# Kernel optimization log

Hardware: AMD Instinct MI355X
Metric: run time of the kernel (lower is better)

Reference implementation:

```python
import jax, jax.numpy as jnp
import numpy as np

N = 64      # num_neighbors + 1
H = 512     # hidden_size
T = 1024    # history length


def setup_inputs() -> dict:
    key = jax.random.key(0)
    ks = jax.random.split(key, 10)
    s = 1.0 / np.sqrt(H)  # PyTorch LSTM/Linear init scale
    return {
        "in_recent_values": jax.random.normal(ks[0], (N,), dtype=jnp.float32),
        "in_reputation_history": jax.random.normal(ks[1], (N, T), dtype=jnp.float32),
        # per-module LSTM params (input_size=1), gate order i,f,g,o
        "W_ih": jax.random.uniform(ks[2], (N, 4 * H), jnp.float32, -s, s),      # [N,4H] (input_size=1 squeezed)
        "W_hh": jax.random.uniform(ks[3], (N, 4 * H, H), jnp.float32, -s, s),   # [N,4H,H]
        "b_ih": jax.random.uniform(ks[4], (N, 4 * H), jnp.float32, -s, s),
        "b_hh": jax.random.uniform(ks[5], (N, 4 * H), jnp.float32, -s, s),
        # per-module output Linear(H+1 -> 1)
        "lin_W": jax.random.uniform(ks[6], (N, H + 1), jnp.float32, -s, s),
        "lin_b": jax.random.uniform(ks[7], (N,), jnp.float32, -s, s),
        # final Linear(N -> 1)
        "final_W": jax.random.uniform(ks[8], (N,), jnp.float32, -1.0 / np.sqrt(N), 1.0 / np.sqrt(N)),
        "final_b": jax.random.uniform(ks[9], (1,), jnp.float32, -1.0 / np.sqrt(N), 1.0 / np.sqrt(N)),
    }


def _batched_lstm_last_h(history, W_ih, W_hh, b_ih, b_hh):
    # history: [N,T]. Precompute input contribution for all steps: [T,N,4H]
    x_proj = history[:, :, None] * W_ih[:, None, :] + (b_ih + b_hh)[:, None, :]
    x_proj = jnp.swapaxes(x_proj, 0, 1)  # [T,N,4H]

    def step(carry, x_t):
        h, c = carry  # [N,H] each
        gates = x_t + jnp.einsum("nh,ngh->ng", h, W_hh)  # [N,4H]
        i, f, g, o = jnp.split(gates, 4, axis=-1)
        i = jax.nn.sigmoid(i)
        f = jax.nn.sigmoid(f)
        g = jnp.tanh(g)
        o = jax.nn.sigmoid(o)
        c = f * c + i * g
        h = o * jnp.tanh(c)
        return (h, c), None

    h0 = jnp.zeros((N, H), dtype=history.dtype)
    (h_last, _), _ = jax.lax.scan(step, (h0, h0), x_proj)
    return h_last  # [N,H]


def reference(in_recent_values, in_reputation_history, W_ih, W_hh, b_ih, b_hh,
              lin_W, lin_b, final_W, final_b):
    h_last = _batched_lstm_last_h(in_reputation_history, W_ih, W_hh, b_ih, b_hh)
    # per-module linear on [h_last, current_reading] -> scalar each
    feat = jnp.concatenate([h_last, in_recent_values[:, None]], axis=1)  # [N,H+1]
    per_mod = jnp.sum(feat * lin_W, axis=1) + lin_b                      # [N]
    out = per_mod @ final_W + final_b                                    # [1]
    return out
```

## Files before the change

### kernel.cpp

```cpp
#include <hip/hip_runtime.h>
#include <hip/hip_fp16.h>
#include <cstddef>

#define NMOD 64
#define HID 512
#define TSTEPS 1024
#define G4 2048

#define WOFF_PERMOD 0
#define WOFF_HX     16384
#define WOFF_W16    524288
#define W16_BYTES   ((size_t)NMOD * G4 * HID * 2)
#define WS_NEED     (WOFF_W16 + W16_BYTES)

typedef _Float16 h2_t __attribute__((ext_vector_type(2)));
union U32H2 { unsigned u; h2_t h; };
__device__ __forceinline__ h2_t u2h(unsigned u) { U32H2 x; x.u = u; return x.h; }

#if __has_builtin(__builtin_amdgcn_fdot2)
#define FDOT2(a, b, c) __builtin_amdgcn_fdot2((a), (b), (c), false)
#else
__device__ __forceinline__ float FDOT2(h2_t a, h2_t b, float c) {
    return c + (float)a[0] * (float)b[0] + (float)a[1] * (float)b[1];
}
#endif

__device__ __forceinline__ float fsig(float x)  { return 1.0f / (1.0f + __expf(-x)); }
__device__ __forceinline__ float ftanh_(float x){ return 1.0f - 2.0f / (__expf(2.0f * x) + 1.0f); }

__global__ __launch_bounds__(256) void conv_kernel(const float* __restrict__ src,
                                                   __half* __restrict__ dst) {
    const size_t i = ((size_t)blockIdx.x * 256 + threadIdx.x) * 8;
    const float4 a = *reinterpret_cast<const float4*>(src + i);
    const float4 b = *reinterpret_cast<const float4*>(src + i + 4);
    __half2 h0 = __floats2half2_rn(a.x, a.y);
    __half2 h1 = __floats2half2_rn(a.z, a.w);
    __half2 h2 = __floats2half2_rn(b.x, b.y);
    __half2 h3 = __floats2half2_rn(b.z, b.w);
    uint4 o;
    o.x = *reinterpret_cast<unsigned*>(&h0);
    o.y = *reinterpret_cast<unsigned*>(&h1);
    o.z = *reinterpret_cast<unsigned*>(&h2);
    o.w = *reinterpret_cast<unsigned*>(&h3);
    *reinterpret_cast<uint4*>(dst + i) = o;
}

__global__ __launch_bounds__(512, 2) void lstm_res_kernel(
    const float* __restrict__ recent,
    const float* __restrict__ history,
    const float* __restrict__ W_ih,
    const float* __restrict__ b_ih,
    const float* __restrict__ b_hh,
    const float* __restrict__ lin_W,
    const float* __restrict__ lin_b,
    const unsigned* __restrict__ w16u,
    unsigned long long* hx,
    float* __restrict__ per_mod)
{
    const int bid = blockIdx.x;
    const int m = (bid & 7) * 8 + ((bid >> 3) >> 2);
    const int b = (bid >> 3) & 3;
    const int tid = threadIdx.x;
    const int rg = tid >> 4;
    const int cg = tid & 15;

    __shared__ unsigned w_lds[32768];
    __shared__ unsigned h_pk[256];
    __shared__ float gates_sh[512];
    __shared__ float hist_sh[TSTEPS];
    __shared__ float red_sh[8];

    for (int i = tid; i < TSTEPS; i += 512)
        hist_sh[i] = history[(size_t)m * TSTEPS + i];

    const size_t rowbase = (size_t)m * G4 * 256;
    uint4 w[12][4];
    #pragma unroll
    for (int r = 0; r < 12; ++r) {
        const int l = rg * 16 + r;
        const int gr = ((l >> 7) << 9) + (b << 7) + (l & 127);
        #pragma unroll
        for (int kk = 0; kk < 4; ++kk) {
            const int c = (((b + kk) & 3) << 4) + cg;
            w[r][kk] = *(const uint4*)(w16u + rowbase + (size_t)gr * 256 + c * 4);
        }
    }
    #pragma unroll
    for (int r2 = 0; r2 < 4; ++r2) {
        const int l = rg * 16 + 12 + r2;
        const int gr = ((l >> 7) << 9) + (b << 7) + (l & 127);
        #pragma unroll
        for (int kk = 0; kk < 4; ++kk) {
            const int c  = (((b + kk) & 3) << 4) + cg;
            const int wc = (((kk + rg) & 3) << 4) + cg;
            *(uint4*)&w_lds[((rg * 4 + r2) * 64 + wc) * 4] =
                *(const uint4*)(w16u + rowbase + (size_t)gr * 256 + c * 4);
        }
    }

    const int rev = ((cg & 1) << 3) | ((cg & 2) << 1) | ((cg & 4) >> 1) | ((cg & 8) >> 3);
    const int l_own = rg * 16 + rev;
    const int gr_own = ((l_own >> 7) << 9) + (b << 7) + (l_own & 127);
    const float wib_own  = W_ih[(size_t)m * G4 + gr_own];
    const float bias_own = b_ih[(size_t)m * G4 + gr_own] + b_hh[(size_t)m * G4 + gr_own];

    const bool is_writer = (tid < 64);
    const bool is_reader = (tid >= 64 && tid < 256);
    const int  rr    = tid - 64;
    const int  widx  = (((b + 1 + (rr >> 6)) & 3) << 6) + (rr & 63);

    float c0 = 0.0f, c1 = 0.0f;

    gates_sh[l_own] = hist_sh[0] * wib_own + bias_own;

    for (int t = 0; t < TSTEPS - 1; ++t) {
        __syncthreads();
        const unsigned seq = (unsigned)(t + 1);
        const size_t pbase = (size_t)(seq & 1) * (NMOD * 256) + (size_t)m * 256;

        unsigned long long pv = 0;
        if (is_writer) {
            const int e0 = 2 * tid, e1 = 2 * tid + 1;
            const float gi0 = fsig(gates_sh[e0]);
            const float gf0 = fsig(gates_sh[128 + e0]);
            const float gg0 = ftanh_(gates_sh[256 + e0]);
            const float go0 = fsig(gates_sh[384 + e0]);
            c0 = gf0 * c0 + gi0 * gg0;
            const float h0 = go0 * ftanh_(c0);
            const float gi1 = fsig(gates_sh[e1]);
            const float gf1 = fsig(gates_sh[128 + e1]);
            const float gg1 = ftanh_(gates_sh[256 + e1]);
            const float go1 = fsig(gates_sh[384 + e1]);
            c1 = gf1 * c1 + gi1 * gg1;
            const float h1 = go1 * ftanh_(c1);
            __half2 hh = __floats2half2_rn(h0, h1);
            const unsigned pay = *reinterpret_cast<unsigned*>(&hh);
            __hip_atomic_store(&hx[pbase + b * 64 + tid],
                               ((unsigned long long)seq << 32) | pay,
                               __ATOMIC_RELAXED, __HIP_MEMORY_SCOPE_AGENT);
            h_pk[b * 64 + tid] = pay;
        } else if (is_reader) {
            pv = __hip_atomic_load(&hx[pbase + widx],
                                   __ATOMIC_RELAXED, __HIP_MEMORY_SCOPE_AGENT);
        }
        __syncthreads();

        float acc[16];
        #pragma unroll
        for (int r = 0; r < 16; ++r) acc[r] = 0.0f;
        {
            const uint4 hq = *(const uint4*)&h_pk[(b << 6) + cg * 4];
            #pragma unroll
            for (int r = 0; r < 12; ++r) {
                acc[r] = FDOT2(u2h(w[r][0].x), u2h(hq.x), acc[r]);
                acc[r] = FDOT2(u2h(w[r][0].y), u2h(hq.y), acc[r]);
                acc[r] = FDOT2(u2h(w[r][0].z), u2h(hq.z), acc[r]);
                acc[r] = FDOT2(u2h(w[r][0].w), u2h(hq.w), acc[r]);
            }
            const int wc0 = ((rg & 3) << 4) + cg;
            #pragma unroll
            for (int r2 = 0; r2 < 4; ++r2) {
                const uint4 lw = *(const uint4*)&w_lds[((rg * 4 + r2) * 64 + wc0) * 4];
                acc[12 + r2] = FDOT2(u2h(lw.x), u2h(hq.x), acc[12 + r2]);
                acc[12 + r2] = FDOT2(u2h(lw.y), u2h(hq.y), acc[12 + r2]);
                acc[12 + r2] = FDOT2(u2h(lw.z), u2h(hq.z), acc[12 + r2]);
                acc[12 + r2] = FDOT2(u2h(lw.w), u2h(hq.w), acc[12 + r2]);
            }
        }

        if (is_reader) {
            while ((unsigned)(pv >> 32) != seq)
                pv = __hip_atomic_load(&hx[pbase + widx],
                                       __ATOMIC_RELAXED, __HIP_MEMORY_SCOPE_AGENT);
            h_pk[widx] = (unsigned)pv;
        }
        __syncthreads();

        #pragma unroll
        for (int kk = 1; kk < 4; ++kk) {
            const uint4 hq = *(const uint4*)&h_pk[((((b + kk) & 3)) << 6) + cg * 4];
            #pragma unroll
            for (int r = 0; r < 12; ++r) {
                acc[r] = FDOT2(u2h(w[r][kk].x), u2h(hq.x), acc[r]);
                acc[r] = FDOT2(u2h(w[r][kk].y), u2h(hq.y), acc[r]);
                acc[r] = FDOT2(u2h(w[r][kk].z), u2h(hq.z), acc[r]);
                acc[r] = FDOT2(u2h(w[r][kk].w), u2h(hq.w), acc[r]);
            }
            const int wc = (((kk + rg) & 3) << 4) + cg;
            #pragma unroll
            for (int r2 = 0; r2 < 4; ++r2) {
                const uint4 lw = *(const uint4*)&w_lds[((rg * 4 + r2) * 64 + wc) * 4];
                acc[12 + r2] = FDOT2(u2h(lw.x), u2h(hq.x), acc[12 + r2]);
                acc[12 + r2] = FDOT2(u2h(lw.y), u2h(hq.y), acc[12 + r2]);
                acc[12 + r2] = FDOT2(u2h(lw.z), u2h(hq.z), acc[12 + r2]);
                acc[12 + r2] = FDOT2(u2h(lw.w), u2h(hq.w), acc[12 + r2]);
            }
        }

        #pragma unroll
        for (int k = 0; k < 8; ++k) {
            const float send = (cg & 1) ? acc[k] : acc[8 + k];
            const float recv = __shfl_xor(send, 1, 64);
            acc[k] = ((cg & 1) ? acc[8 + k] : acc[k]) + recv;
        }
        #pragma unroll
        for (int k = 0; k < 4; ++k) {
            const float send = (cg & 2) ? acc[k] : acc[4 + k];
            const float recv = __shfl_xor(send, 2, 64);
            acc[k] = ((cg & 2) ? acc[4 + k] : acc[k]) + recv;
        }
        #pragma unroll
        for (int k = 0; k < 2; ++k) {
            const float send = (cg & 4) ? acc[k] : acc[2 + k];
            const float recv = __shfl_xor(send, 4, 64);
            acc[k] = ((cg & 4) ? acc[2 + k] : acc[k]) + recv;
        }
        {
            const float send = (cg & 8) ? acc[0] : acc[1];
            const float recv = __shfl_xor(send, 8, 64);
            acc[0] = ((cg & 8) ? acc[1] : acc[0]) + recv;
        }

        gates_sh[l_own] = acc[0] + hist_sh[t + 1] * wib_own + bias_own;
    }

    __syncthreads();
    {
        const unsigned seq = (unsigned)TSTEPS;
        const size_t pbase = (size_t)(seq & 1) * (NMOD * 256) + (size_t)m * 256;
        if (is_writer) {
            const int e0 = 2 * tid, e1 = 2 * tid + 1;
            const float gi0 = fsig(gates_sh[e0]);
            const float gf0 = fsig(gates_sh[128 + e0]);
            const float gg0 = ftanh_(gates_sh[256 + e0]);
            const float go0 = fsig(gates_sh[384 + e0]);
            c0 = gf0 * c0 + gi0 * gg0;
            const float h0 = go0 * ftanh_(c0);
            const float gi1 = fsig(gates_sh[e1]);
            const float gf1 = fsig(gates_sh[128 + e1]);
            const float gg1 = ftanh_(gates_sh[256 + e1]);
            const float go1 = fsig(gates_sh[384 + e1]);
            c1 = gf1 * c1 + gi1 * gg1;
            const float h1 = go1 * ftanh_(c1);
            __half2 hh = __floats2half2_rn(h0, h1);
            const unsigned pay = *reinterpret_cast<unsigned*>(&hh);
            __hip_atomic_store(&hx[pbase + b * 64 + tid],
                               ((unsigned long long)seq << 32) | pay,
                               __ATOMIC_RELAXED, __HIP_MEMORY_SCOPE_AGENT);
            h_pk[b * 64 + tid] = pay;
        }
        if (b == 0) {
            if (is_reader) {
                unsigned long long pv;
                do {
                    pv = __hip_atomic_load(&hx[pbase + widx],
                                           __ATOMIC_RELAXED, __HIP_MEMORY_SCOPE_AGENT);
                } while ((unsigned)(pv >> 32) != seq);
                h_pk[widx] = (unsigned)pv;
            }
            __syncthreads();
            float v = 0.0f;
            if (tid < 256) {
                U32H2 u; u.u = h_pk[tid];
                const float* lwp = lin_W + (size_t)m * (HID + 1);
                v = (float)u.h[0] * lwp[2 * tid] + (float)u.h[1] * lwp[2 * tid + 1];
            }
            #pragma unroll
            for (int s2 = 32; s2; s2 >>= 1) v += __shfl_xor(v, s2, 64);
            if ((tid & 63) == 0) red_sh[tid >> 6] = v;
            __syncthreads();
            if (tid == 0) {
                float s = 0.0f;
                #pragma unroll
                for (int wv2 = 0; wv2 < 8; ++wv2) s += red_sh[wv2];
                s += recent[m] * lin_W[(size_t)m * (HID + 1) + HID] + lin_b[m];
                per_mod[m] = s;
            }
        }
    }
}

__global__ __launch_bounds__(1024) void lstm_module_kernel(
    const float* __restrict__ recent,
    const float* __restrict__ history,
    const float* __restrict__ W_ih,
    const float* __restrict__ W_hh,
    const float* __restrict__ b_ih,
    const float* __restrict__ b_hh,
    const float* __restrict__ lin_W,
    const float* __restrict__ lin_b,
    float* __restrict__ per_mod)
{
    const int n = blockIdx.x;
    const int tid = threadIdx.x;

    __shared__ float h_sh[HID];
    __shared__ float gates_sh[G4];
    __shared__ float wib_sh[G4];
    __shared__ float bias_sh[G4];
    __shared__ float hist_sh[TSTEPS];

    for (int i = tid; i < G4; i += 1024) {
        wib_sh[i]  = W_ih[(size_t)n * G4 + i];
        bias_sh[i] = b_ih[(size_t)n * G4 + i] + b_hh[(size_t)n * G4 + i];
    }
    for (int i = tid; i < TSTEPS; i += 1024) hist_sh[i] = history[(size_t)n * TSTEPS + i];
    if (tid < HID) h_sh[tid] = 0.0f;
    float c_reg = 0.0f;
    __syncthreads();

    const int sub = tid & 15;
    const int rid = tid >> 4;
    const float* Wbase = W_hh + (size_t)n * G4 * HID;

    for (int t = 0; t < TSTEPS; ++t) {
        const float x = hist_sh[t];
        float hreg[32];
        #pragma unroll
        for (int j = 0; j < 8; ++j) {
            const float4 hv = *reinterpret_cast<const float4*>(&h_sh[sub * 4 + j * 64]);
            hreg[4 * j + 0] = hv.x; hreg[4 * j + 1] = hv.y;
            hreg[4 * j + 2] = hv.z; hreg[4 * j + 3] = hv.w;
        }
        for (int p = 0; p < 32; ++p) {
            const int r = p * 64 + rid;
            const float* wr = Wbase + (size_t)r * HID + sub * 4;
            float acc = 0.0f;
            #pragma unroll
            for (int j = 0; j < 8; ++j) {
                const float4 wv = *reinterpret_cast<const float4*>(wr + j * 64);
                acc += wv.x * hreg[4*j+0] + wv.y * hreg[4*j+1]
                     + wv.z * hreg[4*j+2] + wv.w * hreg[4*j+3];
            }
            acc += __shfl_xor(acc, 1, 64);
            acc += __shfl_xor(acc, 2, 64);
            acc += __shfl_xor(acc, 4, 64);
            acc += __shfl_xor(acc, 8, 64);
            if (sub == 0) gates_sh[r] = acc + x * wib_sh[r] + bias_sh[r];
        }
        __syncthreads();
        if (tid < HID) {
            const float ig = fsig(gates_sh[tid]);
            const float fg = fsig(gates_sh[HID + tid]);
            const float gg = ftanh_(gates_sh[2 * HID + tid]);
            const float og = fsig(gates_sh[3 * HID + tid]);
            c_reg = fg * c_reg + ig * gg;
            h_sh[tid] = og * ftanh_(c_reg);
        }
        __syncthreads();
    }

    if (tid < HID) {
        float v = h_sh[tid] * lin_W[(size_t)n * (HID + 1) + tid];
        #pragma unroll
        for (int m2 = 32; m2; m2 >>= 1) v += __shfl_xor(v, m2, 64);
        if ((tid & 63) == 0) gates_sh[tid >> 6] = v;
    }
    __syncthreads();
    if (tid == 0) {
        float s = 0.0f;
        #pragma unroll
        for (int w = 0; w < HID / 64; ++w) s += gates_sh[w];
        s += recent[n] * lin_W[(size_t)n * (HID + 1) + HID] + lin_b[n];
        per_mod[n] = s;
    }
}

__global__ void finish_kernel(const float* __restrict__ per_mod,
                              const float* __restrict__ final_W,
                              const float* __restrict__ final_b,
                              float* __restrict__ out)
{
    const int l = threadIdx.x;
    float v = per_mod[l] * final_W[l];
    #pragma unroll
    for (int m = 32; m; m >>= 1) v += __shfl_xor(v, m, 64);
    if (l == 0) out[0] = v + final_b[0];
}

extern "C" void kernel_launch(void* const* d_in, const int* in_sizes, int n_in,
                              void* d_out, int out_size, void* d_ws, size_t ws_size,
                              hipStream_t stream) {
    const float* recent  = (const float*)d_in[0];
    const float* history = (const float*)d_in[1];
    const float* W_ih    = (const float*)d_in[2];
    const float* W_hh    = (const float*)d_in[3];
    const float* b_ih    = (const float*)d_in[4];
    const float* b_hh    = (const float*)d_in[5];
    const float* lin_W   = (const float*)d_in[6];
    const float* lin_b   = (const float*)d_in[7];
    const float* final_W = (const float*)d_in[8];
    const float* final_b = (const float*)d_in[9];
    float* out = (float*)d_out;
    float* per_mod = (float*)d_ws;

    if (ws_size >= WS_NEED) {
        __half* w16 = (__half*)((char*)d_ws + WOFF_W16);
        unsigned long long* hx = (unsigned long long*)((char*)d_ws + WOFF_HX);

        hipMemsetAsync(d_ws, 0, WOFF_W16, stream);

        const int conv_blocks = (int)((size_t)NMOD * G4 * HID / 8 / 256);
        conv_kernel<<<conv_blocks, 256, 0, stream>>>(W_hh, w16);

        lstm_res_kernel<<<NMOD * 4, 512, 0, stream>>>(
            recent, history, W_ih, b_ih, b_hh, lin_W, lin_b,
            (const unsigned*)w16, hx, per_mod);
    } else {
        lstm_module_kernel<<<NMOD, 1024, 0, stream>>>(
            recent, history, W_ih, W_hh, b_ih, b_hh, lin_W, lin_b, per_mod);
    }
    finish_kernel<<<1, 64, 0, stream>>>(per_mod, final_W, final_b, out);
}
```

Measured before the change: 2.587 ms.

## Spread gate activations over 128 writers and use DPP for reductions

The gate nonlinearity and cell update now run one hidden element per thread across 128 writer threads (two wavefronts) instead of two elements per thread across 64. Lane pairs are combined with a shuffle before the packed fp16 store. The first two butterfly stages of the cross-lane reduction move from ds_bpermute shuffles to DPP quad permutes, and the dot products use inline v_dot2_f32_f16 asm. Reader threads shift to another range, the block-to-module mapping formula is rewritten, and h_pk is zero-initialised. The aim is a shorter serial critical path per timestep, at the cost of an extra shuffle and a second writer wave.

```diff
diff --git a/kernel.cpp b/kernel.cpp
--- a/kernel.cpp
+++ b/kernel.cpp
@@ -13,20 +13,28 @@
 #define W16_BYTES   ((size_t)NMOD * G4 * HID * 2)
 #define WS_NEED     (WOFF_W16 + W16_BYTES)
 
-typedef _Float16 h2_t __attribute__((ext_vector_type(2)));
-union U32H2 { unsigned u; h2_t h; };
-__device__ __forceinline__ h2_t u2h(unsigned u) { U32H2 x; x.u = u; return x.h; }
-
-#if __has_builtin(__builtin_amdgcn_fdot2)
-#define FDOT2(a, b, c) __builtin_amdgcn_fdot2((a), (b), (c), false)
-#else
-__device__ __forceinline__ float FDOT2(h2_t a, h2_t b, float c) {
-    return c + (float)a[0] * (float)b[0] + (float)a[1] * (float)b[1];
-}
-#endif
-
 __device__ __forceinline__ float fsig(float x)  { return 1.0f / (1.0f + __expf(-x)); }
 __device__ __forceinline__ float ftanh_(float x){ return 1.0f - 2.0f / (__expf(2.0f * x) + 1.0f); }
+
+__device__ __forceinline__ float adot2(unsigned a, unsigned b, float c) {
+    float d;
+    asm("v_dot2_f32_f16 %0, %1, %2, %3" : "=v"(d) : "v"(a), "v"(b), "v"(c));
+    return d;
+}
+__device__ __forceinline__ float dot4(uint4 wv, uint4 hv, float acc) {
+    acc = adot2(wv.x, hv.x, acc);
+    acc = adot2(wv.y, hv.y, acc);
+    acc = adot2(wv.z, hv.z, acc);
+    acc = adot2(wv.w, hv.w, acc);
+    return acc;
+}
+
+template<int CTRL>
+__device__ __forceinline__ float dppf(float x) {
+    int xi = __builtin_bit_cast(int, x);
+    int r = __builtin_amdgcn_update_dpp(0, xi, CTRL, 0xF, 0xF, true);
+    return __builtin_bit_cast(float, r);
+}
 
 __global__ __launch_bounds__(256) void conv_kernel(const float* __restrict__ src,
                                                    __half* __restrict__ dst) {
@@ -58,7 +66,7 @@
     float* __restrict__ per_mod)
 {
     const int bid = blockIdx.x;
-    const int m = (bid & 7) * 8 + ((bid >> 3) >> 2);
+    const int m = (bid & 7) * 8 + (bid >> 5);
     const int b = (bid >> 3) & 3;
     const int tid = threadIdx.x;
     const int rg = tid >> 4;
@@ -104,12 +112,14 @@
     const float wib_own  = W_ih[(size_t)m * G4 + gr_own];
     const float bias_own = b_ih[(size_t)m * G4 + gr_own] + b_hh[(size_t)m * G4 + gr_own];
 
-    const bool is_writer = (tid < 64);
-    const bool is_reader = (tid >= 64 && tid < 256);
-    const int  rr    = tid - 64;
+    const bool is_writer = (tid < 128);
+    const bool is_reader = (tid >= 128 && tid < 320);
+    const int  rr    = tid - 128;
     const int  widx  = (((b + 1 + (rr >> 6)) & 3) << 6) + (rr & 63);
 
-    float c0 = 0.0f, c1 = 0.0f;
+    float c0 = 0.0f;
+
+    if (tid < 256) h_pk[tid] = 0u;
 
     gates_sh[l_own] = hist_sh[0] * wib_own + bias_own;
 
@@ -120,25 +130,22 @@
 
         unsigned long long pv = 0;
         if (is_writer) {
-            const int e0 = 2 * tid, e1 = 2 * tid + 1;
-            const float gi0 = fsig(gates_sh[e0]);
-            const float gf0 = fsig(gates_sh[128 + e0]);
-            const float gg0 = ftanh_(gates_sh[256 + e0]);
-            const float go0 = fsig(gates_sh[384 + e0]);
-            c0 = gf0 * c0 + gi0 * gg0;
-            const float h0 = go0 * ftanh_(c0);
-            const float gi1 = fsig(gates_sh[e1]);
-            const float gf1 = fsig(gates_sh[128 + e1]);
-            const float gg1 = ftanh_(gates_sh[256 + e1]);
-            const float go1 = fsig(gates_sh[384 + e1]);
-            c1 = gf1 * c1 + gi1 * gg1;
-            const float h1 = go1 * ftanh_(c1);
-            __half2 hh = __floats2half2_rn(h0, h1);
-            const unsigned pay = *reinterpret_cast<unsigned*>(&hh);
-            __hip_atomic_store(&hx[pbase + b * 64 + tid],
-                               ((unsigned long long)seq << 32) | pay,
-                               __ATOMIC_RELAXED, __HIP_MEMORY_SCOPE_AGENT);
-            h_pk[b * 64 + tid] = pay;
+            const float gi = fsig(gates_sh[tid]);
+            const float gf = fsig(gates_sh[128 + tid]);
+            const float gg = ftanh_(gates_sh[256 + tid]);
+            const float go = fsig(gates_sh[384 + tid]);
+            c0 = gf * c0 + gi * gg;
+            const float hv = go * ftanh_(c0);
+            const float ho = __shfl_xor(hv, 1, 64);
+            if ((tid & 1) == 0) {
+                __half2 hh = __floats2half2_rn(hv, ho);
+                const unsigned pay = *reinterpret_cast<unsigned*>(&hh);
+                const int word = tid >> 1;
+                __hip_atomic_store(&hx[pbase + b * 64 + word],
+                                   ((unsigned long long)seq << 32) | pay,
+                                   __ATOMIC_RELAXED, __HIP_MEMORY_SCOPE_AGENT);
+                h_pk[b * 64 + word] = pay;
+            }
         } else if (is_reader) {
             pv = __hip_atomic_load(&hx[pbase + widx],
                                    __ATOMIC_RELAXED, __HIP_MEMORY_SCOPE_AGENT);
@@ -151,20 +158,12 @@
         {
             const uint4 hq = *(const uint4*)&h_pk[(b << 6) + cg * 4];
             #pragma unroll
-            for (int r = 0; r < 12; ++r) {
-                acc[r] = FDOT2(u2h(w[r][0].x), u2h(hq.x), acc[r]);
-                acc[r] = FDOT2(u2h(w[r][0].y), u2h(hq.y), acc[r]);
-                acc[r] = FDOT2(u2h(w[r][0].z), u2h(hq.z), acc[r]);
-                acc[r] = FDOT2(u2h(w[r][0].w), u2h(hq.w), acc[r]);
-            }
+            for (int r = 0; r < 12; ++r) acc[r] = dot4(w[r][0], hq, acc[r]);
             const int wc0 = ((rg & 3) << 4) + cg;
             #pragma unroll
             for (int r2 = 0; r2 < 4; ++r2) {
                 const uint4 lw = *(const uint4*)&w_lds[((rg * 4 + r2) * 64 + wc0) * 4];
-                acc[12 + r2] = FDOT2(u2h(lw.x), u2h(hq.x), acc[12 + r2]);
-                acc[12 + r2] = FDOT2(u2h(lw.y), u2h(hq.y), acc[12 + r2]);
-                acc[12 + r2] = FDOT2(u2h(lw.z), u2h(hq.z), acc[12 + r2]);
-                acc[12 + r2] = FDOT2(u2h(lw.w), u2h(hq.w), acc[12 + r2]);
+                acc[12 + r2] = dot4(lw, hq, acc[12 + r2]);
             }
         }
 
@@ -180,33 +179,25 @@
         for (int kk = 1; kk < 4; ++kk) {
             const uint4 hq = *(const uint4*)&h_pk[((((b + kk) & 3)) << 6) + cg * 4];
             #pragma unroll
-            for (int r = 0; r < 12; ++r) {
-                acc[r] = FDOT2(u2h(w[r][kk].x), u2h(hq.x), acc[r]);
-                acc[r] = FDOT2(u2h(w[r][kk].y), u2h(hq.y), acc[r]);
-                acc[r] = FDOT2(u2h(w[r][kk].z), u2h(hq.z), acc[r]);
-                acc[r] = FDOT2(u2h(w[r][kk].w), u2h(hq.w), acc[r]);
-            }
+            for (int r = 0; r < 12; ++r) acc[r] = dot4(w[r][kk], hq, acc[r]);
             const int wc = (((kk + rg) & 3) << 4) + cg;
             #pragma unroll
             for (int r2 = 0; r2 < 4; ++r2) {
                 const uint4 lw = *(const uint4*)&w_lds[((rg * 4 + r2) * 64 + wc) * 4];
-                acc[12 + r2] = FDOT2(u2h(lw.x), u2h(hq.x), acc[12 + r2]);
-                acc[12 + r2] = FDOT2(u2h(lw.y), u2h(hq.y), acc[12 + r2]);
-                acc[12 + r2] = FDOT2(u2h(lw.z), u2h(hq.z), acc[12 + r2]);
-                acc[12 + r2] = FDOT2(u2h(lw.w), u2h(hq.w), acc[12 + r2]);
+                acc[12 + r2] = dot4(lw, hq, acc[12 + r2]);
             }
         }
 
         #pragma unroll
         for (int k = 0; k < 8; ++k) {
             const float send = (cg & 1) ? acc[k] : acc[8 + k];
-            const float recv = __shfl_xor(send, 1, 64);
+            const float recv = dppf<0xB1>(send);
             acc[k] = ((cg & 1) ? acc[8 + k] : acc[k]) + recv;
         }
         #pragma unroll
         for (int k = 0; k < 4; ++k) {
             const float send = (cg & 2) ? acc[k] : acc[4 + k];
-            const float recv = __shfl_xor(send, 2, 64);
+            const float recv = dppf<0x4E>(send);
             acc[k] = ((cg & 2) ? acc[4 + k] : acc[k]) + recv;
         }
         #pragma unroll
@@ -229,25 +220,22 @@
         const unsigned seq = (unsigned)TSTEPS;
         const size_t pbase = (size_t)(seq & 1) * (NMOD * 256) + (size_t)m * 256;
         if (is_writer) {
-            const int e0 = 2 * tid, e1 = 2 * tid + 1;
-            const float gi0 = fsig(gates_sh[e0]);
-            const float gf0 = fsig(gates_sh[128 + e0]);
-            const float gg0 = ftanh_(gates_sh[256 + e0]);
-            const float go0 = fsig(gates_sh[384 + e0]);
-            c0 = gf0 * c0 + gi0 * gg0;
-            const float h0 = go0 * ftanh_(c0);
-            const float gi1 = fsig(gates_sh[e1]);
-            const float gf1 = fsig(gates_sh[128 + e1]);
-            const float gg1 = ftanh_(gates_sh[256 + e1]);
-            const float go1 = fsig(gates_sh[384 + e1]);
-            c1 = gf1 * c1 + gi1 * gg1;
-            const float h1 = go1 * ftanh_(c1);
-            __half2 hh = __floats2half2_rn(h0, h1);
-            const unsigned pay = *reinterpret_cast<unsigned*>(&hh);
-            __hip_atomic_store(&hx[pbase + b * 64 + tid],
-                               ((unsigned long long)seq << 32) | pay,
-                               __ATOMIC_RELAXED, __HIP_MEMORY_SCOPE_AGENT);
-            h_pk[b * 64 + tid] = pay;
+            const float gi = fsig(gates_sh[tid]);
+            const float gf = fsig(gates_sh[128 + tid]);
+            const float gg = ftanh_(gates_sh[256 + tid]);
+            const float go = fsig(gates_sh[384 + tid]);
+            c0 = gf * c0 + gi * gg;
+            const float hv = go * ftanh_(c0);
+            const float ho = __shfl_xor(hv, 1, 64);
+            if ((tid & 1) == 0) {
+                __half2 hh = __floats2half2_rn(hv, ho);
+                const unsigned pay = *reinterpret_cast<unsigned*>(&hh);
+                const int word = tid >> 1;
+                __hip_atomic_store(&hx[pbase + b * 64 + word],
+                                   ((unsigned long long)seq << 32) | pay,
+                                   __ATOMIC_RELAXED, __HIP_MEMORY_SCOPE_AGENT);
+                h_pk[b * 64 + word] = pay;
+            }
         }
         if (b == 0) {
             if (is_reader) {
@@ -261,9 +249,9 @@
             __syncthreads();
             float v = 0.0f;
             if (tid < 256) {
-                U32H2 u; u.u = h_pk[tid];
+                const __half2 u = *reinterpret_cast<const __half2*>(&h_pk[tid]);
                 const float* lwp = lin_W + (size_t)m * (HID + 1);
-                v = (float)u.h[0] * lwp[2 * tid] + (float)u.h[1] * lwp[2 * tid + 1];
+                v = __half2float(u.x) * lwp[2 * tid] + __half2float(u.y) * lwp[2 * tid + 1];
             }
             #pragma unroll
             for (int s2 = 32; s2; s2 >>= 1) v += __shfl_xor(v, s2, 64);
```

Result: faster. 2.440 ms (-5.7%).
